# Kernel optimization log

Hardware: AMD Instinct MI355X
Metric: run time of the kernel (lower is better)

## Reference

```python
import jax, jax.numpy as jnp
import numpy as np

# config matching init_kwargs
SW_SIZE = 512       # signal_window_size
SUBW = 256          # subwindow_size
NSW = 2             # subwindow_nbins = time_points // subwindow_size
DCT_NBINS = 8
NDCT = SUBW // DCT_NBINS   # 32, also nfreqs
NF = 64             # dct_num_filters
SLOPE = 0.02        # LeakyReLU negative slope
HW = 8


def dct2_mat(N):
    # torch_dct.dct with norm=None: X_k = 2 * sum_n x_n cos(pi*(2n+1)*k/(2N))
    n = jnp.arange(N, dtype=jnp.float32)
    k = jnp.arange(N, dtype=jnp.float32)
    return 2.0 * jnp.cos(jnp.pi * (2.0 * n[None, :] + 1.0) * k[:, None] / (2.0 * N))


def setup_inputs() -> dict:
    key = jax.random.key(0)
    k1, k2, k3 = jax.random.split(key, 3)
    x = jax.random.normal(k1, (1024, 1, SW_SIZE, HW, HW), dtype=jnp.float32)
    W = jax.random.normal(k2, (NSW, NF, NDCT, HW, HW), dtype=jnp.float32) * 0.02
    b = jax.random.normal(k3, (NSW, NF), dtype=jnp.float32) * 0.02
    return {"x": x, "W": W, "b": b}


def reference(x, W, b):
    B = x.shape[0]
    # time_slice_interval=1 and maxpool=1 are identity.
    # split time into (subwindows, dct bins, ndct points): [B, NSW, DCT_NBINS, NDCT, 8, 8]
    xs = x[:, 0].reshape(B, NSW, DCT_NBINS, NDCT, HW, HW)
    Ct = dct2_mat(NDCT)
    Cs = dct2_mat(HW)
    # dct_3d: DCT-II along last three dims (time-in-bin, H, W)
    y = jnp.einsum('ft,bsctij->bscfij', Ct, xs)
    y = jnp.einsum('pi,bscfij->bscfpj', Cs, y)
    y = jnp.einsum('qj,bscfpj->bscfpq', Cs, y)
    # mean over dct bins -> [B, NSW, NDCT, 8, 8]
    m = jnp.mean(y, axis=2)
    # per-subwindow full-receptive-field Conv3d == dot product -> [B, NSW, NF]
    feat = jnp.einsum('bsfpq,sofpq->bso', m, W) + b[None, :, :]
    # dropout is identity (eval / rate 0); LeakyReLU then flatten from dim 1
    feat = jnp.where(feat >= 0, feat, SLOPE * feat)
    return feat.reshape(B, -1)
```

## Files before the change

kernel.cpp:

```cpp
#include <hip/hip_runtime.h>

#define NSW 2
#define NDCT 32
#define NF 64
#define KDIM 2048
#define SLOPE 0.02f
#define PI_F 3.14159265358979323846f

__global__ __launch_bounds__(256) void veff_kernel(const float* __restrict__ W,
                                                   float* __restrict__ Veff) {
    __shared__ float Ct[32][32];
    __shared__ float Cs[8][8];
    __shared__ float bufA[2048];
    __shared__ float bufB[2048];
    const int tid = threadIdx.x;

    for (int idx = tid; idx < 1024; idx += 256) {
        int f = idx >> 5, t = idx & 31;
        Ct[f][t] = 2.0f * cosf(PI_F * (float)((2 * t + 1) * f) * (1.0f / 64.0f));
    }
    if (tid < 64) {
        int p = tid >> 3, i = tid & 7;
        Cs[p][i] = 2.0f * cosf(PI_F * (float)((2 * i + 1) * p) * (1.0f / 16.0f));
    }
    const float* Wso = W + blockIdx.x * 2048;
    for (int idx = tid; idx < 2048; idx += 256) bufA[idx] = Wso[idx];
    __syncthreads();

    for (int idx = tid; idx < 2048; idx += 256) {
        int t = idx >> 6, pq = idx & 63;
        float s = 0.f;
        #pragma unroll
        for (int f = 0; f < 32; ++f) s += Ct[f][t] * bufA[f * 64 + pq];
        bufB[idx] = s;
    }
    __syncthreads();

    for (int idx = tid; idx < 2048; idx += 256) {
        int t = idx >> 6, i = (idx >> 3) & 7, q = idx & 7;
        float s = 0.f;
        #pragma unroll
        for (int p = 0; p < 8; ++p) s += Cs[p][i] * bufB[t * 64 + p * 8 + q];
        bufA[idx] = s;
    }
    __syncthreads();

    for (int idx = tid; idx < 2048; idx += 256) {
        int t = idx >> 6, i = (idx >> 3) & 7, j = idx & 7;
        float s = 0.f;
        #pragma unroll
        for (int q = 0; q < 8; ++q) s += Cs[q][j] * bufA[t * 64 + i * 8 + q];
        Veff[blockIdx.x * 2048 + idx] = 0.125f * s;
    }
}

__global__ __launch_bounds__(256) void reduce_c_kernel(const float* __restrict__ x,
                                                       float* __restrict__ xsum) {
    int g = blockIdx.x * 256 + threadIdx.x;
    int ij4 = g & 15;
    int t   = (g >> 4) & 31;
    int s   = (g >> 9) & 1;
    int b   = g >> 10;
    const float4* xp = (const float4*)x + ((b * 512 + s * 256 + t) * 16 + ij4);
    float4 acc = make_float4(0.f, 0.f, 0.f, 0.f);
    #pragma unroll
    for (int c = 0; c < 8; ++c) {
        float4 v = xp[c * 32 * 16];
        acc.x += v.x; acc.y += v.y; acc.z += v.z; acc.w += v.w;
    }
    ((float4*)xsum)[g] = acc;
}

__global__ __launch_bounds__(256) void gemm_kernel(const float* __restrict__ xsum,
                                                   const float* __restrict__ Veff,
                                                   const float* __restrict__ bias,
                                                   float* __restrict__ out) {
    __shared__ float4 Vs4[64 * 65];
    __shared__ float4 Xs4[4 * 64];
    __shared__ float  part[4][4][64];
    const int s   = blockIdx.y;
    const int b0  = blockIdx.x * 4;
    const int tid = threadIdx.x;
    const int o   = tid & 63;
    const int kq  = tid >> 6;

    const float4* xsum4 = (const float4*)xsum;
    const float4* Veff4 = (const float4*)Veff;

    float acc0 = 0.f, acc1 = 0.f, acc2 = 0.f, acc3 = 0.f;

    for (int kt = 0; kt < 8; ++kt) {
        __syncthreads();
        #pragma unroll
        for (int j = 0; j < 16; ++j) {
            int idx = tid + j * 256;
            int oo = idx >> 6, k4 = idx & 63;
            Vs4[oo * 65 + k4] = Veff4[(s * 64 + oo) * 512 + kt * 64 + k4];
        }
        {
            int b = tid >> 6, k4 = tid & 63;
            Xs4[tid] = xsum4[((b0 + b) * 2 + s) * 512 + kt * 64 + k4];
        }
        __syncthreads();
        #pragma unroll
        for (int m = 0; m < 16; ++m) {
            int k4 = kq * 16 + m;
            float4 v  = Vs4[o * 65 + k4];
            float4 x0 = Xs4[0 * 64 + k4];
            float4 x1 = Xs4[1 * 64 + k4];
            float4 x2 = Xs4[2 * 64 + k4];
            float4 x3 = Xs4[3 * 64 + k4];
            acc0 += v.x * x0.x + v.y * x0.y + v.z * x0.z + v.w * x0.w;
            acc1 += v.x * x1.x + v.y * x1.y + v.z * x1.z + v.w * x1.w;
            acc2 += v.x * x2.x + v.y * x2.y + v.z * x2.z + v.w * x2.w;
            acc3 += v.x * x3.x + v.y * x3.y + v.z * x3.z + v.w * x3.w;
        }
    }

    part[kq][0][o] = acc0;
    part[kq][1][o] = acc1;
    part[kq][2][o] = acc2;
    part[kq][3][o] = acc3;
    __syncthreads();
    {
        int b = tid >> 6, oo = tid & 63;
        float f = part[0][b][oo] + part[1][b][oo] + part[2][b][oo] + part[3][b][oo]
                + bias[s * 64 + oo];
        f = (f >= 0.f) ? f : SLOPE * f;
        out[(b0 + b) * 128 + s * 64 + oo] = f;
    }
}

extern "C" void kernel_launch(void* const* d_in, const int* in_sizes, int n_in,
                              void* d_out, int out_size, void* d_ws, size_t ws_size,
                              hipStream_t stream) {
    const float* x    = (const float*)d_in[0];
    const float* W    = (const float*)d_in[1];
    const float* bias = (const float*)d_in[2];
    float* out = (float*)d_out;

    const int B = in_sizes[0] / (512 * 64);

    float* Veff = (float*)d_ws;
    float* xsum = Veff + NSW * NF * KDIM;

    veff_kernel<<<NSW * NF, 256, 0, stream>>>(W, Veff);

    int n4 = B * NSW * NDCT * 16;
    reduce_c_kernel<<<n4 / 256, 256, 0, stream>>>(x, xsum);

    gemm_kernel<<<dim3(B / 4, NSW), 256, 0, stream>>>(xsum, Veff, bias, out);
}
```

Baseline: 227.2 us.

## Fuse DCT-bin reduction into GEMM kernel to drop xsum round trip

Merges the bin-summing reduce kernel into the GEMM kernel: each block sums the 8 DCT bins for its 4 batches and one subwindow straight from x into shared memory (32 KB), then runs the dot product against Veff. The k-tile is halved to 32 float4s so the Veff staging buffer fits next to the larger X buffer. This removes the xsum write and re-read through global memory and one kernel launch. In exchange, shared memory per block grows, which may lower occupancy, and the loads of x are now done by only 512 blocks instead of a wide grid, so memory-level parallelism may drop.

```diff
diff --git a/kernel.cpp b/kernel.cpp
--- a/kernel.cpp
+++ b/kernel.cpp
@@ -35,7 +35,6 @@
         bufB[idx] = s;
     }
     __syncthreads();
-
     for (int idx = tid; idx < 2048; idx += 256) {
         int t = idx >> 6, i = (idx >> 3) & 7, q = idx & 7;
         float s = 0.f;
@@ -44,7 +43,6 @@
         bufA[idx] = s;
     }
     __syncthreads();
-
     for (int idx = tid; idx < 2048; idx += 256) {
         int t = idx >> 6, i = (idx >> 3) & 7, j = idx & 7;
         float s = 0.f;
@@ -54,62 +52,56 @@
     }
 }
 
-__global__ __launch_bounds__(256) void reduce_c_kernel(const float* __restrict__ x,
-                                                       float* __restrict__ xsum) {
-    int g = blockIdx.x * 256 + threadIdx.x;
-    int ij4 = g & 15;
-    int t   = (g >> 4) & 31;
-    int s   = (g >> 9) & 1;
-    int b   = g >> 10;
-    const float4* xp = (const float4*)x + ((b * 512 + s * 256 + t) * 16 + ij4);
-    float4 acc = make_float4(0.f, 0.f, 0.f, 0.f);
-    #pragma unroll
-    for (int c = 0; c < 8; ++c) {
-        float4 v = xp[c * 32 * 16];
-        acc.x += v.x; acc.y += v.y; acc.z += v.z; acc.w += v.w;
-    }
-    ((float4*)xsum)[g] = acc;
-}
-
-__global__ __launch_bounds__(256) void gemm_kernel(const float* __restrict__ xsum,
-                                                   const float* __restrict__ Veff,
-                                                   const float* __restrict__ bias,
-                                                   float* __restrict__ out) {
-    __shared__ float4 Vs4[64 * 65];
-    __shared__ float4 Xs4[4 * 64];
+__global__ __launch_bounds__(256) void fused_kernel(const float* __restrict__ x,
+                                                    const float* __restrict__ Veff,
+                                                    const float* __restrict__ bias,
+                                                    float* __restrict__ out) {
+    __shared__ float4 Xs4[4 * 512];
+    __shared__ float4 Vs4[64 * 33];
     __shared__ float  part[4][4][64];
     const int s   = blockIdx.y;
     const int b0  = blockIdx.x * 4;
     const int tid = threadIdx.x;
-    const int o   = tid & 63;
-    const int kq  = tid >> 6;
 
-    const float4* xsum4 = (const float4*)xsum;
-    const float4* Veff4 = (const float4*)Veff;
+    const float4* xbase = (const float4*)x;
+    #pragma unroll
+    for (int b = 0; b < 4; ++b) {
+        #pragma unroll
+        for (int r = 0; r < 2; ++r) {
+            int k4 = tid + r * 256;
+            const float4* xp = xbase + (((size_t)(b0 + b) * 512 + s * 256) * 16 + k4);
+            float4 acc = make_float4(0.f, 0.f, 0.f, 0.f);
+            #pragma unroll
+            for (int c = 0; c < 8; ++c) {
+                float4 v = xp[c * 512];
+                acc.x += v.x; acc.y += v.y; acc.z += v.z; acc.w += v.w;
+            }
+            Xs4[b * 512 + k4] = acc;
+        }
+    }
+
+    const int o  = tid & 63;
+    const int kq = tid >> 6;
+    const float4* Veff4 = (const float4*)Veff + (size_t)s * 64 * 512;
 
     float acc0 = 0.f, acc1 = 0.f, acc2 = 0.f, acc3 = 0.f;
-
-    for (int kt = 0; kt < 8; ++kt) {
+    for (int kt = 0; kt < 16; ++kt) {
         __syncthreads();
         #pragma unroll
-        for (int j = 0; j < 16; ++j) {
+        for (int j = 0; j < 8; ++j) {
             int idx = tid + j * 256;
-            int oo = idx >> 6, k4 = idx & 63;
-            Vs4[oo * 65 + k4] = Veff4[(s * 64 + oo) * 512 + kt * 64 + k4];
-        }
-        {
-            int b = tid >> 6, k4 = tid & 63;
-            Xs4[tid] = xsum4[((b0 + b) * 2 + s) * 512 + kt * 64 + k4];
+            int oo = idx >> 5, k4 = idx & 31;
+            Vs4[oo * 33 + k4] = Veff4[oo * 512 + kt * 32 + k4];
         }
         __syncthreads();
         #pragma unroll
-        for (int m = 0; m < 16; ++m) {
-            int k4 = kq * 16 + m;
-            float4 v  = Vs4[o * 65 + k4];
-            float4 x0 = Xs4[0 * 64 + k4];
-            float4 x1 = Xs4[1 * 64 + k4];
-            float4 x2 = Xs4[2 * 64 + k4];
-            float4 x3 = Xs4[3 * 64 + k4];
+        for (int m = 0; m < 8; ++m) {
+            int k4 = kq * 8 + m;
+            float4 v  = Vs4[o * 33 + k4];
+            float4 x0 = Xs4[0 * 512 + kt * 32 + k4];
+            float4 x1 = Xs4[1 * 512 + kt * 32 + k4];
+            float4 x2 = Xs4[2 * 512 + kt * 32 + k4];
+            float4 x3 = Xs4[3 * 512 + kt * 32 + k4];
             acc0 += v.x * x0.x + v.y * x0.y + v.z * x0.z + v.w * x0.w;
             acc1 += v.x * x1.x + v.y * x1.y + v.z * x1.z + v.w * x1.w;
             acc2 += v.x * x2.x + v.y * x2.y + v.z * x2.z + v.w * x2.w;
@@ -127,7 +119,7 @@
         float f = part[0][b][oo] + part[1][b][oo] + part[2][b][oo] + part[3][b][oo]
                 + bias[s * 64 + oo];
         f = (f >= 0.f) ? f : SLOPE * f;
-        out[(b0 + b) * 128 + s * 64 + oo] = f;
+        out[(size_t)(b0 + b) * 128 + s * 64 + oo] = f;
     }
 }
 
@@ -142,12 +134,7 @@
     const int B = in_sizes[0] / (512 * 64);
 
     float* Veff = (float*)d_ws;
-    float* xsum = Veff + NSW * NF * KDIM;
 
     veff_kernel<<<NSW * NF, 256, 0, stream>>>(W, Veff);
-
-    int n4 = B * NSW * NDCT * 16;
-    reduce_c_kernel<<<n4 / 256, 256, 0, stream>>>(x, xsum);
-
-    gemm_kernel<<<dim3(B / 4, NSW), 256, 0, stream>>>(xsum, Veff, bias, out);
+    fused_kernel<<<dim3(B / 4, NSW), 256, 0, stream>>>(x, Veff, bias, out);
 }
```

New measurement: 220.3 us. -3.0%, faster.
